# Performance work log

Measured on AMD Instinct MI355X. Metric: run time of the kernel, lower is better.

## Reference

```python
import jax, jax.numpy as jnp
import numpy as np

EPS = 1e-12  # matches torch euclidean_dist clamp(min=1e-12)


def _euclidean_dist(a, b):
    # pairwise sqrt distances: [N, M]
    d2 = (jnp.sum(a * a, axis=1)[:, None]
          + jnp.sum(b * b, axis=1)[None, :]
          - 2.0 * (a @ b.T))
    return jnp.sqrt(jnp.clip(d2, EPS))


def setup_inputs() -> dict:
    key = jax.random.key(0)
    k1, k2, k3 = jax.random.split(key, 3)
    B, I, E, C = 131072, 512, 128, 64
    x = jax.random.normal(k1, (B, I), dtype=jnp.float32)
    y = jax.random.randint(k2, (B,), 0, C)  # class labels
    W = jax.random.normal(k3, (E, I), dtype=jnp.float32) * 0.02
    b = jnp.zeros((E,), dtype=jnp.float32)
    centroid = jnp.zeros((C, E), dtype=jnp.float32)
    return {"x": x, "y": y, "W": W, "b": b, "centroid": centroid}


def reference(x, y, W, b, centroid):
    # linear projection: [B, E]
    out = x @ W.T + b
    C = centroid.shape[0]
    # fused per-class masked mean (segment mean). flag[i]==0 always in the
    # original module, so the executed update is centroid[i] += mean_i.
    sums = jax.ops.segment_sum(out, y, num_segments=C)            # [C, E]
    counts = jax.ops.segment_sum(jnp.ones(y.shape, out.dtype), y,
                                 num_segments=C)                   # [C]
    means = sums / counts[:, None]
    new_centroid = centroid + means
    # only the final loop iteration's proto_dist / dist survive
    proto_dist = jnp.exp(-0.5 * _euclidean_dist(new_centroid, new_centroid))
    dist = _euclidean_dist(out, new_centroid)                      # [B, C]
    return jax.nn.sigmoid(jnp.exp(-0.5 * dist)), proto_dist
```

## Files before the change

### kernel.cpp

```cpp
#include <hip/hip_runtime.h>
#include <math.h>


typedef __bf16 bf16;
typedef bf16  bf16x2 __attribute__((ext_vector_type(2)));
typedef bf16  bf16x4 __attribute__((ext_vector_type(4)));
typedef bf16  bf16x8 __attribute__((ext_vector_type(8)));
typedef float f32x4  __attribute__((ext_vector_type(4)));

#define B_ROWS 131072
#define K_DIM  512
#define E_DIM  128
#define C_CLS  64

#define BM 128
#define BK 64

#define SEG_BLOCKS 512
#define ROWS_PER_SEG (B_ROWS / SEG_BLOCKS)

#define DIST_BLOCKS (B_ROWS / 128)
#define PROTO_BLOCKS 16

__global__ __launch_bounds__(256, 2)
void gemm_kernel(const float* __restrict__ x, const float* __restrict__ W,
                 const float* __restrict__ bias, bf16* __restrict__ outb,
                 float* __restrict__ rnorm)
{
    __shared__ bf16 As[2][BM * BK];
    __shared__ bf16 Bs[2][BM * BK];
    __shared__ float lr[BM];

    const int t    = threadIdx.x;
    const int lane = t & 63;
    const int w    = t >> 6;
    const int wr   = w >> 1;
    const int wc   = w & 1;
    const int fr   = lane & 15;
    const int fq   = lane >> 4;
    const long blockRow = (long)blockIdx.x * BM;

    const int srow = t >> 4;
    const int scol = (t & 15) * 4;

    f32x4 acc[4][4] = {};
    f32x4 va[8], vb[8];

    const float* xg = x + blockRow * K_DIM;
    if (t < BM) lr[t] = 0.f;

    #pragma unroll
    for (int r = 0; r < 8; ++r) {
        int row = r * 16 + srow;
        va[r] = *(const f32x4*)(xg + (long)row * K_DIM + scol);
        vb[r] = *(const f32x4*)(W  + (long)row * K_DIM + scol);
    }
    #pragma unroll
    for (int r = 0; r < 8; ++r) {
        int row = r * 16 + srow;
        bf16x4 pa = { (bf16)va[r].x, (bf16)va[r].y, (bf16)va[r].z, (bf16)va[r].w };
        bf16x4 pb = { (bf16)vb[r].x, (bf16)vb[r].y, (bf16)vb[r].z, (bf16)vb[r].w };
        int byte = row * (BK * 2) + ((scol * 2) ^ ((row & 7) << 4));
        *(bf16x4*)((char*)As[0] + byte) = pa;
        *(bf16x4*)((char*)Bs[0] + byte) = pb;
    }
    __syncthreads();

    for (int kti = 0; kti < K_DIM / BK; ++kti) {
        const int p = kti & 1;
        if (kti < K_DIM / BK - 1) {
            const int kt = (kti + 1) * BK;
            #pragma unroll
            for (int r = 0; r < 8; ++r) {
                int row = r * 16 + srow;
                va[r] = *(const f32x4*)(xg + (long)row * K_DIM + kt + scol);
                vb[r] = *(const f32x4*)(W  + (long)row * K_DIM + kt + scol);
            }
        }
        const bf16* Ap = As[p];
        const bf16* Bp = Bs[p];
        #pragma unroll
        for (int kk = 0; kk < 2; ++kk) {
            bf16x8 af[4], bg[4];
            #pragma unroll
            for (int m = 0; m < 4; ++m) {
                int row  = wr * 64 + m * 16 + fr;
                int byte = row * (BK * 2) + (((kk * 32 + fq * 8) * 2) ^ ((row & 7) << 4));
                af[m] = *(const bf16x8*)((const char*)Ap + byte);
            }
            #pragma unroll
            for (int n = 0; n < 4; ++n) {
                int row  = wc * 64 + n * 16 + fr;
                int byte = row * (BK * 2) + (((kk * 32 + fq * 8) * 2) ^ ((row & 7) << 4));
                bg[n] = *(const bf16x8*)((const char*)Bp + byte);
            }
            #pragma unroll
            for (int m = 0; m < 4; ++m)
                #pragma unroll
                for (int n = 0; n < 4; ++n)
                    acc[m][n] = __builtin_amdgcn_mfma_f32_16x16x32_bf16(
                        af[m], bg[n], acc[m][n], 0, 0, 0);
        }
        if (kti < K_DIM / BK - 1) {
            #pragma unroll
            for (int r = 0; r < 8; ++r) {
                int row = r * 16 + srow;
                bf16x4 pa = { (bf16)va[r].x, (bf16)va[r].y, (bf16)va[r].z, (bf16)va[r].w };
                bf16x4 pb = { (bf16)vb[r].x, (bf16)vb[r].y, (bf16)vb[r].z, (bf16)vb[r].w };
                int byte = row * (BK * 2) + ((scol * 2) ^ ((row & 7) << 4));
                *(bf16x4*)((char*)As[p ^ 1] + byte) = pa;
                *(bf16x4*)((char*)Bs[p ^ 1] + byte) = pb;
            }
            __syncthreads();
        }
    }

    float bvv[4];
    #pragma unroll
    for (int n = 0; n < 4; ++n) bvv[n] = bias[wc * 64 + n * 16 + fr];

    #pragma unroll
    for (int m = 0; m < 4; ++m) {
        #pragma unroll
        for (int j = 0; j < 4; ++j) {
            long grow = blockRow + wr * 64 + m * 16 + fq * 4 + j;
            float s = 0.f;
            #pragma unroll
            for (int n = 0; n < 4; ++n) {
                float v = acc[m][n][j] + bvv[n];
                outb[grow * E_DIM + wc * 64 + n * 16 + fr] = (bf16)v;
                s += v * v;
            }
            s += __shfl_xor(s, 1); s += __shfl_xor(s, 2);
            s += __shfl_xor(s, 4); s += __shfl_xor(s, 8);
            if (fr == 0) atomicAdd(&lr[wr * 64 + m * 16 + fq * 4 + j], s);
        }
    }
    __syncthreads();
    if (t < BM) rnorm[blockRow + t] = lr[t];
}

__global__ __launch_bounds__(256)
void segsum_kernel(const bf16* __restrict__ outb, const int* __restrict__ y,
                   float* __restrict__ pw, float* __restrict__ pc)
{
    __shared__ float lsum[C_CLS * E_DIM];
    __shared__ float lcnt[C_CLS];
    __shared__ int   ly[ROWS_PER_SEG];
    const int t = threadIdx.x;
    for (int i = t; i < C_CLS * E_DIM; i += 256) lsum[i] = 0.f;
    if (t < C_CLS) lcnt[t] = 0.f;
    const long base = (long)blockIdx.x * ROWS_PER_SEG;
    if (t < ROWS_PER_SEG) ly[t] = y[base + t];
    __syncthreads();
    const int w = t >> 6, lane = t & 63;
    #pragma unroll 4
    for (int i = w; i < ROWS_PER_SEG; i += 4) {
        int cls = ly[i];
        bf16x2 v = *(const bf16x2*)(outb + (base + i) * E_DIM + lane * 2);
        atomicAdd(&lsum[cls * E_DIM + lane * 2 + 0], (float)v[0]);
        atomicAdd(&lsum[cls * E_DIM + lane * 2 + 1], (float)v[1]);
        if (lane == 0) atomicAdd(&lcnt[cls], 1.f);
    }
    __syncthreads();
    for (int i = t; i < C_CLS * E_DIM; i += 256)
        pw[(long)blockIdx.x * (C_CLS * E_DIM) + i] = lsum[i];
    if (t < C_CLS) pc[blockIdx.x * C_CLS + t] = lcnt[t];
}

__global__ __launch_bounds__(256)
void reduce_kernel(const float* __restrict__ pw, float* __restrict__ sums)
{
    __shared__ float red[256];
    const int t = threadIdx.x;
    const int idx = blockIdx.x * 32 + (t & 31);
    const int js  = t >> 5;
    float s = 0.f;
    #pragma unroll 8
    for (int j = js * 64; j < js * 64 + 64; ++j)
        s += pw[(long)j * (C_CLS * E_DIM) + idx];
    red[t] = s;
    __syncthreads();
    if (t < 32) {
        float r = red[t];
        #pragma unroll
        for (int k = 1; k < 8; ++k) r += red[t + 32 * k];
        sums[blockIdx.x * 32 + t] = r;
    }
}

__global__ __launch_bounds__(256)
void centroid_kernel(const float* __restrict__ sums, const float* __restrict__ pc,
                     const float* __restrict__ centroid0,
                     float* __restrict__ cent, float* __restrict__ cnorm)
{
    __shared__ float red[256];
    const int c = blockIdx.x;
    const int t = threadIdx.x;
    float s = pc[t * C_CLS + c] + pc[(t + 256) * C_CLS + c];
    red[t] = s;
    __syncthreads();
    #pragma unroll
    for (int st = 128; st > 0; st >>= 1) {
        if (t < st) red[t] += red[t + st];
        __syncthreads();
    }
    const float cnt = red[0];
    __syncthreads();
    float v = 0.f;
    if (t < E_DIM) {
        v = centroid0[c * E_DIM + t] + sums[c * E_DIM + t] / cnt;
        cent[c * E_DIM + t] = v;
    }
    red[t] = v * v;
    __syncthreads();
    #pragma unroll
    for (int st = 64; st > 0; st >>= 1) {
        if (t < st) red[t] += red[t + st];
        __syncthreads();
    }
    if (t == 0) cnorm[c] = red[0];
}

__global__ __launch_bounds__(256, 4)
void dist_kernel(const bf16* __restrict__ outb, const float* __restrict__ cent,
                 const float* __restrict__ cnorm, const float* __restrict__ rnorm,
                 float* __restrict__ out0, float* __restrict__ proto)
{
    __shared__ float smemf[C_CLS * 129 + C_CLS + 128];
    const int t = threadIdx.x;

    if (blockIdx.x >= DIST_BLOCKS) {
        float* scf   = smemf;
        float* pnorm = smemf + C_CLS * 129;
        for (int idx = t; idx < C_CLS * E_DIM; idx += 256)
            scf[(idx >> 7) * 129 + (idx & 127)] = cent[idx];
        if (t < C_CLS) pnorm[t] = cnorm[t];
        __syncthreads();
        int p = (blockIdx.x - DIST_BLOCKS) * 256 + t;
        int i = p >> 6, j = p & 63;
        float d = 0.f;
        #pragma unroll 4
        for (int e = 0; e < E_DIM; ++e)
            d += scf[i * 129 + e] * scf[j * 129 + e];
        float d2 = pnorm[i] + pnorm[j] - 2.f * d;
        proto[p] = __expf(-0.5f * sqrtf(fmaxf(d2, 1e-12f)));
        return;
    }

    bf16*  Cs     = (bf16*)smemf;
    float* snorm  = smemf + C_CLS * 129;
    float* srnorm = snorm + C_CLS;
    {
        int srw = t >> 5;
        int scl = (t & 31) * 4;
        #pragma unroll
        for (int r = 0; r < 8; ++r) {
            int row = r * 8 + srw;
            f32x4 v = *(const f32x4*)(cent + row * E_DIM + scl);
            bf16x4 pv = { (bf16)v.x, (bf16)v.y, (bf16)v.z, (bf16)v.w };
            int byte = row * (E_DIM * 2) + ((scl * 2) ^ ((row & 7) << 4));
            *(bf16x4*)((char*)Cs + byte) = pv;
        }
        if (t < C_CLS) snorm[t] = cnorm[t];
        if (t < 32) ((f32x4*)srnorm)[t] =
            ((const f32x4*)(rnorm + (long)blockIdx.x * 128))[t];
    }
    const int lane = t & 63;
    const int w    = t >> 6;
    const int fr   = lane & 15;
    const int fq   = lane >> 4;
    const long blkrow = (long)blockIdx.x * 128;
    f32x4 acc[2][4] = {};
    __syncthreads();
    #pragma unroll
    for (int kt = 0; kt < 4; ++kt) {
        bf16x8 af[2];
        #pragma unroll
        for (int m = 0; m < 2; ++m) {
            long row = blkrow + w * 32 + m * 16 + fr;
            af[m] = *(const bf16x8*)(outb + row * E_DIM + kt * 32 + fq * 8);
        }
        #pragma unroll
        for (int n = 0; n < 4; ++n) {
            int row  = n * 16 + fr;
            int byte = row * (E_DIM * 2) + (((kt * 32 + fq * 8) * 2) ^ ((row & 7) << 4));
            bf16x8 bq = *(const bf16x8*)((const char*)Cs + byte);
            acc[0][n] = __builtin_amdgcn_mfma_f32_16x16x32_bf16(af[0], bq, acc[0][n], 0, 0, 0);
            acc[1][n] = __builtin_amdgcn_mfma_f32_16x16x32_bf16(af[1], bq, acc[1][n], 0, 0, 0);
        }
    }
    #pragma unroll
    for (int m = 0; m < 2; ++m) {
        #pragma unroll
        for (int n = 0; n < 4; ++n) {
            int gcol = n * 16 + fr;
            float cn = snorm[gcol];
            #pragma unroll
            for (int j = 0; j < 4; ++j) {
                int lrow = w * 32 + m * 16 + fq * 4 + j;
                float d2 = srnorm[lrow] + cn - 2.f * acc[m][n][j];
                float dist = sqrtf(fmaxf(d2, 1e-12f));
                float ez = __expf(-0.5f * dist);
                out0[(blkrow + lrow) * C_CLS + gcol] = 1.f / (1.f + __expf(-ez));
            }
        }
    }
}

extern "C" void kernel_launch(void* const* d_in, const int* in_sizes, int n_in,
                              void* d_out, int out_size, void* d_ws, size_t ws_size,
                              hipStream_t stream)
{
    const float* x         = (const float*)d_in[0];
    const int*   y         = (const int*)d_in[1];
    const float* W         = (const float*)d_in[2];
    const float* bias      = (const float*)d_in[3];
    const float* centroid0 = (const float*)d_in[4];

    bf16*  outb  = (bf16*)d_ws;
    float* rnorm = (float*)((char*)d_ws + (size_t)B_ROWS * E_DIM * 2);
    float* pw    = rnorm + B_ROWS;
    float* pc    = pw + (long)SEG_BLOCKS * C_CLS * E_DIM;
    float* sums  = pc + SEG_BLOCKS * C_CLS;
    float* cent  = sums + C_CLS * E_DIM;
    float* cnorm = cent + C_CLS * E_DIM;

    float* out0  = (float*)d_out;
    float* proto = out0 + (long)B_ROWS * C_CLS;

    gemm_kernel    <<<B_ROWS / BM, 256, 0, stream>>>(x, W, bias, outb, rnorm);
    segsum_kernel  <<<SEG_BLOCKS, 256, 0, stream>>>(outb, y, pw, pc);
    reduce_kernel  <<<(C_CLS * E_DIM) / 32, 256, 0, stream>>>(pw, sums);
    centroid_kernel<<<C_CLS, 256, 0, stream>>>(sums, pc, centroid0, cent, cnorm);
    dist_kernel    <<<DIST_BLOCKS + PROTO_BLOCKS, 256, 0, stream>>>(
        outb, cent, cnorm, rnorm, out0, proto);
}
```

Measured before the change: 194.7 us.

## Fuse all stages into one persistent kernel with software grid barriers

Replaces the five-kernel pipeline with a single persistent kernel of 512 blocks that runs GEMM, segment sum, reduction, centroid update and distance stages, separated by atomic-counter grid barriers. Each block handles two GEMM tiles and two distance tiles, and the centroid and norm computation is done redundantly in every block. The aim is to remove launch gaps and the small serial kernels. The risks are that GEMM occupancy falls to 512 blocks (a 64KB static LDS allocation), that barrier spinning adds cost, and that progress depends on all blocks being co-resident.

Result: slower. 416.8 us (+114.1%).

```diff
diff --git a/kernel.cpp b/kernel.cpp
--- a/kernel.cpp
+++ b/kernel.cpp
@@ -16,294 +16,282 @@
 #define BM 128
 #define BK 64
 
-#define SEG_BLOCKS 512
-#define ROWS_PER_SEG (B_ROWS / SEG_BLOCKS)
-
-#define DIST_BLOCKS (B_ROWS / 128)
-#define PROTO_BLOCKS 16
+#define GRID 512
+#define ROWS_PER_SEG (B_ROWS / GRID)
+
+__device__ __forceinline__ void grid_sync(unsigned* bar, unsigned target)
+{
+    __syncthreads();
+    if (threadIdx.x == 0) {
+        __threadfence();
+        atomicAdd(bar, 1u);
+        while (atomicAdd(bar, 0u) < target)
+            __builtin_amdgcn_s_sleep(16);
+    }
+    __syncthreads();
+    __threadfence();
+}
 
 __global__ __launch_bounds__(256, 2)
-void gemm_kernel(const float* __restrict__ x, const float* __restrict__ W,
-                 const float* __restrict__ bias, bf16* __restrict__ outb,
-                 float* __restrict__ rnorm)
+void mega_kernel(const float* __restrict__ x, const int* __restrict__ y,
+                 const float* __restrict__ W, const float* __restrict__ bias,
+                 const float* __restrict__ centroid0,
+                 bf16* __restrict__ outb, float* __restrict__ rnorm,
+                 float* __restrict__ pw, float* __restrict__ pc,
+                 float* __restrict__ sums, float* __restrict__ cntg,
+                 float* __restrict__ out0, float* __restrict__ proto,
+                 unsigned* __restrict__ bar)
 {
-    __shared__ bf16 As[2][BM * BK];
-    __shared__ bf16 Bs[2][BM * BK];
-    __shared__ float lr[BM];
-
+    __shared__ __align__(16) char smem[65536];
     const int t    = threadIdx.x;
     const int lane = t & 63;
     const int w    = t >> 6;
-    const int wr   = w >> 1;
-    const int wc   = w & 1;
-    const int fr   = lane & 15;
-    const int fq   = lane >> 4;
-    const long blockRow = (long)blockIdx.x * BM;
-
-    const int srow = t >> 4;
-    const int scol = (t & 15) * 4;
-
-    f32x4 acc[4][4] = {};
-    f32x4 va[8], vb[8];
-
-    const float* xg = x + blockRow * K_DIM;
-    if (t < BM) lr[t] = 0.f;
-
-    #pragma unroll
-    for (int r = 0; r < 8; ++r) {
-        int row = r * 16 + srow;
-        va[r] = *(const f32x4*)(xg + (long)row * K_DIM + scol);
-        vb[r] = *(const f32x4*)(W  + (long)row * K_DIM + scol);
-    }
-    #pragma unroll
-    for (int r = 0; r < 8; ++r) {
-        int row = r * 16 + srow;
-        bf16x4 pa = { (bf16)va[r].x, (bf16)va[r].y, (bf16)va[r].z, (bf16)va[r].w };
-        bf16x4 pb = { (bf16)vb[r].x, (bf16)vb[r].y, (bf16)vb[r].z, (bf16)vb[r].w };
-        int byte = row * (BK * 2) + ((scol * 2) ^ ((row & 7) << 4));
-        *(bf16x4*)((char*)As[0] + byte) = pa;
-        *(bf16x4*)((char*)Bs[0] + byte) = pb;
-    }
-    __syncthreads();
-
-    for (int kti = 0; kti < K_DIM / BK; ++kti) {
-        const int p = kti & 1;
-        if (kti < K_DIM / BK - 1) {
-            const int kt = (kti + 1) * BK;
+
+    {
+        bf16* As = (bf16*)smem;
+        bf16* Bs = (bf16*)(smem + 32768);
+        const int wr = w >> 1, wc = w & 1;
+        const int fr = lane & 15, fq = lane >> 4;
+        const int srow = t >> 4;
+        const int scol = (t & 15) * 4;
+
+        for (int rep = 0; rep < 2; ++rep) {
+            const int  tile = blockIdx.x + rep * GRID;
+            const long blockRow = (long)tile * BM;
+            const float* xg = x + blockRow * K_DIM;
+            f32x4 acc[4][4] = {};
+            f32x4 va[8], vb[8];
+
+            __syncthreads();
             #pragma unroll
             for (int r = 0; r < 8; ++r) {
                 int row = r * 16 + srow;
-                va[r] = *(const f32x4*)(xg + (long)row * K_DIM + kt + scol);
-                vb[r] = *(const f32x4*)(W  + (long)row * K_DIM + kt + scol);
-            }
-        }
-        const bf16* Ap = As[p];
-        const bf16* Bp = Bs[p];
-        #pragma unroll
-        for (int kk = 0; kk < 2; ++kk) {
-            bf16x8 af[4], bg[4];
-            #pragma unroll
-            for (int m = 0; m < 4; ++m) {
-                int row  = wr * 64 + m * 16 + fr;
-                int byte = row * (BK * 2) + (((kk * 32 + fq * 8) * 2) ^ ((row & 7) << 4));
-                af[m] = *(const bf16x8*)((const char*)Ap + byte);
-            }
-            #pragma unroll
-            for (int n = 0; n < 4; ++n) {
-                int row  = wc * 64 + n * 16 + fr;
-                int byte = row * (BK * 2) + (((kk * 32 + fq * 8) * 2) ^ ((row & 7) << 4));
-                bg[n] = *(const bf16x8*)((const char*)Bp + byte);
-            }
-            #pragma unroll
-            for (int m = 0; m < 4; ++m)
-                #pragma unroll
-                for (int n = 0; n < 4; ++n)
-                    acc[m][n] = __builtin_amdgcn_mfma_f32_16x16x32_bf16(
-                        af[m], bg[n], acc[m][n], 0, 0, 0);
-        }
-        if (kti < K_DIM / BK - 1) {
+                va[r] = *(const f32x4*)(xg + (long)row * K_DIM + scol);
+                vb[r] = *(const f32x4*)(W  + (long)row * K_DIM + scol);
+            }
             #pragma unroll
             for (int r = 0; r < 8; ++r) {
                 int row = r * 16 + srow;
                 bf16x4 pa = { (bf16)va[r].x, (bf16)va[r].y, (bf16)va[r].z, (bf16)va[r].w };
                 bf16x4 pb = { (bf16)vb[r].x, (bf16)vb[r].y, (bf16)vb[r].z, (bf16)vb[r].w };
                 int byte = row * (BK * 2) + ((scol * 2) ^ ((row & 7) << 4));
-                *(bf16x4*)((char*)As[p ^ 1] + byte) = pa;
-                *(bf16x4*)((char*)Bs[p ^ 1] + byte) = pb;
-            }
-            __syncthreads();
-        }
-    }
-
-    float bvv[4];
-    #pragma unroll
-    for (int n = 0; n < 4; ++n) bvv[n] = bias[wc * 64 + n * 16 + fr];
-
-    #pragma unroll
-    for (int m = 0; m < 4; ++m) {
-        #pragma unroll
-        for (int j = 0; j < 4; ++j) {
-            long grow = blockRow + wr * 64 + m * 16 + fq * 4 + j;
-            float s = 0.f;
-            #pragma unroll
-            for (int n = 0; n < 4; ++n) {
-                float v = acc[m][n][j] + bvv[n];
-                outb[grow * E_DIM + wc * 64 + n * 16 + fr] = (bf16)v;
-                s += v * v;
-            }
-            s += __shfl_xor(s, 1); s += __shfl_xor(s, 2);
-            s += __shfl_xor(s, 4); s += __shfl_xor(s, 8);
-            if (fr == 0) atomicAdd(&lr[wr * 64 + m * 16 + fq * 4 + j], s);
-        }
-    }
-    __syncthreads();
-    if (t < BM) rnorm[blockRow + t] = lr[t];
-}
-
-__global__ __launch_bounds__(256)
-void segsum_kernel(const bf16* __restrict__ outb, const int* __restrict__ y,
-                   float* __restrict__ pw, float* __restrict__ pc)
-{
-    __shared__ float lsum[C_CLS * E_DIM];
-    __shared__ float lcnt[C_CLS];
-    __shared__ int   ly[ROWS_PER_SEG];
-    const int t = threadIdx.x;
-    for (int i = t; i < C_CLS * E_DIM; i += 256) lsum[i] = 0.f;
-    if (t < C_CLS) lcnt[t] = 0.f;
-    const long base = (long)blockIdx.x * ROWS_PER_SEG;
-    if (t < ROWS_PER_SEG) ly[t] = y[base + t];
-    __syncthreads();
-    const int w = t >> 6, lane = t & 63;
-    #pragma unroll 4
-    for (int i = w; i < ROWS_PER_SEG; i += 4) {
-        int cls = ly[i];
-        bf16x2 v = *(const bf16x2*)(outb + (base + i) * E_DIM + lane * 2);
-        atomicAdd(&lsum[cls * E_DIM + lane * 2 + 0], (float)v[0]);
-        atomicAdd(&lsum[cls * E_DIM + lane * 2 + 1], (float)v[1]);
-        if (lane == 0) atomicAdd(&lcnt[cls], 1.f);
-    }
-    __syncthreads();
-    for (int i = t; i < C_CLS * E_DIM; i += 256)
-        pw[(long)blockIdx.x * (C_CLS * E_DIM) + i] = lsum[i];
-    if (t < C_CLS) pc[blockIdx.x * C_CLS + t] = lcnt[t];
-}
-
-__global__ __launch_bounds__(256)
-void reduce_kernel(const float* __restrict__ pw, float* __restrict__ sums)
-{
-    __shared__ float red[256];
-    const int t = threadIdx.x;
-    const int idx = blockIdx.x * 32 + (t & 31);
-    const int js  = t >> 5;
-    float s = 0.f;
-    #pragma unroll 8
-    for (int j = js * 64; j < js * 64 + 64; ++j)
-        s += pw[(long)j * (C_CLS * E_DIM) + idx];
-    red[t] = s;
-    __syncthreads();
-    if (t < 32) {
-        float r = red[t];
-        #pragma unroll
-        for (int k = 1; k < 8; ++k) r += red[t + 32 * k];
-        sums[blockIdx.x * 32 + t] = r;
-    }
-}
-
-__global__ __launch_bounds__(256)
-void centroid_kernel(const float* __restrict__ sums, const float* __restrict__ pc,
-                     const float* __restrict__ centroid0,
-                     float* __restrict__ cent, float* __restrict__ cnorm)
-{
-    __shared__ float red[256];
-    const int c = blockIdx.x;
-    const int t = threadIdx.x;
-    float s = pc[t * C_CLS + c] + pc[(t + 256) * C_CLS + c];
-    red[t] = s;
-    __syncthreads();
-    #pragma unroll
-    for (int st = 128; st > 0; st >>= 1) {
-        if (t < st) red[t] += red[t + st];
-        __syncthreads();
-    }
-    const float cnt = red[0];
-    __syncthreads();
-    float v = 0.f;
-    if (t < E_DIM) {
-        v = centroid0[c * E_DIM + t] + sums[c * E_DIM + t] / cnt;
-        cent[c * E_DIM + t] = v;
-    }
-    red[t] = v * v;
-    __syncthreads();
-    #pragma unroll
-    for (int st = 64; st > 0; st >>= 1) {
-        if (t < st) red[t] += red[t + st];
-        __syncthreads();
-    }
-    if (t == 0) cnorm[c] = red[0];
-}
-
-__global__ __launch_bounds__(256, 4)
-void dist_kernel(const bf16* __restrict__ outb, const float* __restrict__ cent,
-                 const float* __restrict__ cnorm, const float* __restrict__ rnorm,
-                 float* __restrict__ out0, float* __restrict__ proto)
-{
-    __shared__ float smemf[C_CLS * 129 + C_CLS + 128];
-    const int t = threadIdx.x;
-
-    if (blockIdx.x >= DIST_BLOCKS) {
-        float* scf   = smemf;
-        float* pnorm = smemf + C_CLS * 129;
-        for (int idx = t; idx < C_CLS * E_DIM; idx += 256)
-            scf[(idx >> 7) * 129 + (idx & 127)] = cent[idx];
-        if (t < C_CLS) pnorm[t] = cnorm[t];
-        __syncthreads();
-        int p = (blockIdx.x - DIST_BLOCKS) * 256 + t;
-        int i = p >> 6, j = p & 63;
-        float d = 0.f;
+                *(bf16x4*)((char*)As + byte) = pa;
+                *(bf16x4*)((char*)Bs + byte) = pb;
+            }
+            __syncthreads();
+
+            for (int kti = 0; kti < K_DIM / BK; ++kti) {
+                const int p = kti & 1;
+                if (kti < K_DIM / BK - 1) {
+                    const int kt = (kti + 1) * BK;
+                    #pragma unroll
+                    for (int r = 0; r < 8; ++r) {
+                        int row = r * 16 + srow;
+                        va[r] = *(const f32x4*)(xg + (long)row * K_DIM + kt + scol);
+                        vb[r] = *(const f32x4*)(W  + (long)row * K_DIM + kt + scol);
+                    }
+                }
+                const char* Ap = (const char*)As + p * 16384;
+                const char* Bp = (const char*)Bs + p * 16384;
+                #pragma unroll
+                for (int kk = 0; kk < 2; ++kk) {
+                    bf16x8 af[4], bg[4];
+                    #pragma unroll
+                    for (int m = 0; m < 4; ++m) {
+                        int row  = wr * 64 + m * 16 + fr;
+                        int byte = row * (BK * 2) + (((kk * 32 + fq * 8) * 2) ^ ((row & 7) << 4));
+                        af[m] = *(const bf16x8*)(Ap + byte);
+                    }
+                    #pragma unroll
+                    for (int n = 0; n < 4; ++n) {
+                        int row  = wc * 64 + n * 16 + fr;
+                        int byte = row * (BK * 2) + (((kk * 32 + fq * 8) * 2) ^ ((row & 7) << 4));
+                        bg[n] = *(const bf16x8*)(Bp + byte);
+                    }
+                    #pragma unroll
+                    for (int m = 0; m < 4; ++m)
+                        #pragma unroll
+                        for (int n = 0; n < 4; ++n)
+                            acc[m][n] = __builtin_amdgcn_mfma_f32_16x16x32_bf16(
+                                af[m], bg[n], acc[m][n], 0, 0, 0);
+                }
+                if (kti < K_DIM / BK - 1) {
+                    #pragma unroll
+                    for (int r = 0; r < 8; ++r) {
+                        int row = r * 16 + srow;
+                        bf16x4 pa = { (bf16)va[r].x, (bf16)va[r].y, (bf16)va[r].z, (bf16)va[r].w };
+                        bf16x4 pb = { (bf16)vb[r].x, (bf16)vb[r].y, (bf16)vb[r].z, (bf16)vb[r].w };
+                        int byte = row * (BK * 2) + ((scol * 2) ^ ((row & 7) << 4));
+                        *(bf16x4*)((char*)As + (p ^ 1) * 16384 + byte) = pa;
+                        *(bf16x4*)((char*)Bs + (p ^ 1) * 16384 + byte) = pb;
+                    }
+                    __syncthreads();
+                }
+            }
+
+            __syncthreads();
+            float* lr = (float*)smem;
+            if (t < BM) lr[t] = 0.f;
+            __syncthreads();
+            float bvv[4];
+            #pragma unroll
+            for (int n = 0; n < 4; ++n) bvv[n] = bias[wc * 64 + n * 16 + fr];
+            #pragma unroll
+            for (int m = 0; m < 4; ++m) {
+                #pragma unroll
+                for (int j = 0; j < 4; ++j) {
+                    long grow = blockRow + wr * 64 + m * 16 + fq * 4 + j;
+                    float s = 0.f;
+                    #pragma unroll
+                    for (int n = 0; n < 4; ++n) {
+                        float v = acc[m][n][j] + bvv[n];
+                        outb[grow * E_DIM + wc * 64 + n * 16 + fr] = (bf16)v;
+                        s += v * v;
+                    }
+                    s += __shfl_xor(s, 1); s += __shfl_xor(s, 2);
+                    s += __shfl_xor(s, 4); s += __shfl_xor(s, 8);
+                    if (fr == 0) atomicAdd(&lr[wr * 64 + m * 16 + fq * 4 + j], s);
+                }
+            }
+            __syncthreads();
+            if (t < BM) rnorm[blockRow + t] = lr[t];
+        }
+    }
+    grid_sync(bar, GRID);
+
+    {
+        float* lsum = (float*)smem;
+        float* lcnt = (float*)(smem + 32768);
+        int*   ly   = (int*)(smem + 33024);
+        for (int i = t; i < C_CLS * E_DIM; i += 256) lsum[i] = 0.f;
+        if (t < C_CLS) lcnt[t] = 0.f;
+        const long base = (long)blockIdx.x * ROWS_PER_SEG;
+        if (t < ROWS_PER_SEG) ly[t] = y[base + t];
+        __syncthreads();
         #pragma unroll 4
-        for (int e = 0; e < E_DIM; ++e)
-            d += scf[i * 129 + e] * scf[j * 129 + e];
-        float d2 = pnorm[i] + pnorm[j] - 2.f * d;
-        proto[p] = __expf(-0.5f * sqrtf(fmaxf(d2, 1e-12f)));
-        return;
-    }
-
-    bf16*  Cs     = (bf16*)smemf;
-    float* snorm  = smemf + C_CLS * 129;
-    float* srnorm = snorm + C_CLS;
+        for (int i = w; i < ROWS_PER_SEG; i += 4) {
+            int cls = ly[i];
+            bf16x2 v = *(const bf16x2*)(outb + (base + i) * E_DIM + lane * 2);
+            atomicAdd(&lsum[cls * E_DIM + lane * 2 + 0], (float)v[0]);
+            atomicAdd(&lsum[cls * E_DIM + lane * 2 + 1], (float)v[1]);
+            if (lane == 0) atomicAdd(&lcnt[cls], 1.f);
+        }
+        __syncthreads();
+        for (int i = t; i < C_CLS * E_DIM; i += 256)
+            pw[(long)blockIdx.x * (C_CLS * E_DIM) + i] = lsum[i];
+        if (t < C_CLS) pc[blockIdx.x * C_CLS + t] = lcnt[t];
+    }
+    grid_sync(bar, 2 * GRID);
+
     {
-        int srw = t >> 5;
-        int scl = (t & 31) * 4;
-        #pragma unroll
-        for (int r = 0; r < 8; ++r) {
-            int row = r * 8 + srw;
-            f32x4 v = *(const f32x4*)(cent + row * E_DIM + scl);
-            bf16x4 pv = { (bf16)v.x, (bf16)v.y, (bf16)v.z, (bf16)v.w };
-            int byte = row * (E_DIM * 2) + ((scl * 2) ^ ((row & 7) << 4));
-            *(bf16x4*)((char*)Cs + byte) = pv;
-        }
-        if (t < C_CLS) snorm[t] = cnorm[t];
-        if (t < 32) ((f32x4*)srnorm)[t] =
-            ((const f32x4*)(rnorm + (long)blockIdx.x * 128))[t];
-    }
-    const int lane = t & 63;
-    const int w    = t >> 6;
-    const int fr   = lane & 15;
-    const int fq   = lane >> 4;
-    const long blkrow = (long)blockIdx.x * 128;
-    f32x4 acc[2][4] = {};
-    __syncthreads();
-    #pragma unroll
-    for (int kt = 0; kt < 4; ++kt) {
-        bf16x8 af[2];
-        #pragma unroll
-        for (int m = 0; m < 2; ++m) {
-            long row = blkrow + w * 32 + m * 16 + fr;
-            af[m] = *(const bf16x8*)(outb + row * E_DIM + kt * 32 + fq * 8);
-        }
-        #pragma unroll
-        for (int n = 0; n < 4; ++n) {
-            int row  = n * 16 + fr;
-            int byte = row * (E_DIM * 2) + (((kt * 32 + fq * 8) * 2) ^ ((row & 7) << 4));
-            bf16x8 bq = *(const bf16x8*)((const char*)Cs + byte);
-            acc[0][n] = __builtin_amdgcn_mfma_f32_16x16x32_bf16(af[0], bq, acc[0][n], 0, 0, 0);
-            acc[1][n] = __builtin_amdgcn_mfma_f32_16x16x32_bf16(af[1], bq, acc[1][n], 0, 0, 0);
-        }
-    }
-    #pragma unroll
-    for (int m = 0; m < 2; ++m) {
-        #pragma unroll
-        for (int n = 0; n < 4; ++n) {
-            int gcol = n * 16 + fr;
-            float cn = snorm[gcol];
-            #pragma unroll
-            for (int j = 0; j < 4; ++j) {
-                int lrow = w * 32 + m * 16 + fq * 4 + j;
-                float d2 = srnorm[lrow] + cn - 2.f * acc[m][n][j];
-                float dist = sqrtf(fmaxf(d2, 1e-12f));
-                float ez = __expf(-0.5f * dist);
-                out0[(blkrow + lrow) * C_CLS + gcol] = 1.f / (1.f + __expf(-ez));
-            }
+        float* scr = (float*)smem;
+        const int i16 = t & 15, slice = t >> 4;
+        const int idx = blockIdx.x * 16 + i16;
+        float s = 0.f;
+        #pragma unroll 8
+        for (int j = slice * 32; j < slice * 32 + 32; ++j)
+            s += pw[(long)j * (C_CLS * E_DIM) + idx];
+        scr[slice * 16 + i16] = s;
+        __syncthreads();
+        if (t < 16) {
+            float r = 0.f;
+            #pragma unroll
+            for (int k = 0; k < 16; ++k) r += scr[k * 16 + t];
+            sums[blockIdx.x * 16 + t] = r;
+        }
+        if (blockIdx.x < C_CLS) {
+            __syncthreads();
+            int c = blockIdx.x;
+            scr[t] = pc[t * C_CLS + c] + pc[(t + 256) * C_CLS + c];
+            __syncthreads();
+            for (int st = 128; st > 0; st >>= 1) {
+                if (t < st) scr[t] += scr[t + st];
+                __syncthreads();
+            }
+            if (t == 0) cntg[c] = scr[0];
+        }
+    }
+    grid_sync(bar, 3 * GRID);
+
+    {
+        float* centf  = (float*)smem;
+        float* cnormS = (float*)(smem + 33024);
+        bf16*  Cs     = (bf16*)(smem + 33280);
+        float* srn    = (float*)(smem + 49664);
+        float* scr2   = (float*)(smem + 50176);
+
+        for (int i = t; i < C_CLS * E_DIM; i += 256) {
+            int cc = i >> 7, e = i & 127;
+            float v = centroid0[i] + sums[i] / cntg[cc];
+            centf[cc * 129 + e] = v;
+            int byte = cc * 256 + ((e * 2) ^ ((cc & 7) << 4));
+            *(bf16*)((char*)Cs + byte) = (bf16)v;
+        }
+        __syncthreads();
+        {
+            int c = t >> 2, q = t & 3;
+            float sSum = 0.f;
+            #pragma unroll 8
+            for (int e = q * 32; e < q * 32 + 32; ++e) {
+                float v = centf[c * 129 + e];
+                sSum += v * v;
+            }
+            scr2[t] = sSum;
+        }
+        __syncthreads();
+        if (t < C_CLS)
+            cnormS[t] = scr2[4 * t] + scr2[4 * t + 1] + scr2[4 * t + 2] + scr2[4 * t + 3];
+
+        const int fr = lane & 15, fq = lane >> 4;
+        for (int rep = 0; rep < 2; ++rep) {
+            const long blkrow = (long)(blockIdx.x + rep * GRID) * 128;
+            __syncthreads();
+            if (t < 32) ((f32x4*)srn)[t] = ((const f32x4*)(rnorm + blkrow))[t];
+            __syncthreads();
+            f32x4 acc[2][4] = {};
+            #pragma unroll
+            for (int kt = 0; kt < 4; ++kt) {
+                bf16x8 af[2];
+                #pragma unroll
+                for (int m = 0; m < 2; ++m) {
+                    long row = blkrow + w * 32 + m * 16 + fr;
+                    af[m] = *(const bf16x8*)(outb + row * E_DIM + kt * 32 + fq * 8);
+                }
+                #pragma unroll
+                for (int n = 0; n < 4; ++n) {
+                    int row  = n * 16 + fr;
+                    int byte = row * (E_DIM * 2) + (((kt * 32 + fq * 8) * 2) ^ ((row & 7) << 4));
+                    bf16x8 bq = *(const bf16x8*)((const char*)Cs + byte);
+                    acc[0][n] = __builtin_amdgcn_mfma_f32_16x16x32_bf16(af[0], bq, acc[0][n], 0, 0, 0);
+                    acc[1][n] = __builtin_amdgcn_mfma_f32_16x16x32_bf16(af[1], bq, acc[1][n], 0, 0, 0);
+                }
+            }
+            #pragma unroll
+            for (int m = 0; m < 2; ++m) {
+                #pragma unroll
+                for (int n = 0; n < 4; ++n) {
+                    int gcol = n * 16 + fr;
+                    float cn = cnormS[gcol];
+                    #pragma unroll
+                    for (int j = 0; j < 4; ++j) {
+                        int lrow = w * 32 + m * 16 + fq * 4 + j;
+                        float d2 = srn[lrow] + cn - 2.f * acc[m][n][j];
+                        float dist = sqrtf(fmaxf(d2, 1e-12f));
+                        float ez = __expf(-0.5f * dist);
+                        out0[(blkrow + lrow) * C_CLS + gcol] = 1.f / (1.f + __expf(-ez));
+                    }
+                }
+            }
+        }
+        if (blockIdx.x < 16) {
+            int p = blockIdx.x * 256 + t;
+            int i = p >> 6, j = p & 63;
+            float d = 0.f;
+            #pragma unroll 4
+            for (int e = 0; e < E_DIM; ++e)
+                d += centf[i * 129 + e] * centf[j * 129 + e];
+            float d2 = cnormS[i] + cnormS[j] - 2.f * d;
+            proto[p] = __expf(-0.5f * sqrtf(fmaxf(d2, 1e-12f)));
         }
     }
 }
@@ -318,21 +306,20 @@
     const float* bias      = (const float*)d_in[3];
     const float* centroid0 = (const float*)d_in[4];
 
-    bf16*  outb  = (bf16*)d_ws;
-    float* rnorm = (float*)((char*)d_ws + (size_t)B_ROWS * E_DIM * 2);
-    float* pw    = rnorm + B_ROWS;
-    float* pc    = pw + (long)SEG_BLOCKS * C_CLS * E_DIM;
-    float* sums  = pc + SEG_BLOCKS * C_CLS;
-    float* cent  = sums + C_CLS * E_DIM;
-    float* cnorm = cent + C_CLS * E_DIM;
+    char* ws = (char*)d_ws;
+    bf16*  outb  = (bf16*)ws;
+    float* rnorm = (float*)(ws + 33554432);
+    float* pw    = (float*)(ws + 34078720);
+    float* pc    = (float*)(ws + 50855936);
+    float* sums  = (float*)(ws + 50987008);
+    float* cntg  = (float*)(ws + 51019776);
+    unsigned* bar = (unsigned*)(ws + 51020032);
 
     float* out0  = (float*)d_out;
     float* proto = out0 + (long)B_ROWS * C_CLS;
 
-    gemm_kernel    <<<B_ROWS / BM, 256, 0, stream>>>(x, W, bias, outb, rnorm);
-    segsum_kernel  <<<SEG_BLOCKS, 256, 0, stream>>>(outb, y, pw, pc);
-    reduce_kernel  <<<(C_CLS * E_DIM) / 32, 256, 0, stream>>>(pw, sums);
-    centroid_kernel<<<C_CLS, 256, 0, stream>>>(sums, pc, centroid0, cent, cnorm);
-    dist_kernel    <<<DIST_BLOCKS + PROTO_BLOCKS, 256, 0, stream>>>(
-        outb, cent, cnorm, rnorm, out0, proto);
+    hipMemsetAsync(bar, 0, 64, stream);
+    hipLaunchKernelGGL(mega_kernel, dim3(GRID), dim3(256), 0, stream,
+                       x, y, W, bias, centroid0,
+                       outb, rnorm, pw, pc, sums, cntg, out0, proto, bar);
 }
```

## Fuse class segment-sum into GEMM epilogue and merge reduction into centroid kernel

Applied to the files above, without the earlier changes.

The GEMM kernel now processes two row tiles per block and, in its epilogue, accumulates per-class sums and counts into shared memory, writing per-tile partials. This removes the separate segsum pass that re-read the projected activations, plus the reduce kernel. The centroid kernel now reduces all 1024 partials directly. In exchange, partial-buffer writes double, the final reduction runs on only 64 blocks, and shared-memory atomics in the epilogue may contend.

Measured after the change: 299.2 us. 1.54x slower.

```diff
diff --git a/kernel.cpp b/kernel.cpp
--- a/kernel.cpp
+++ b/kernel.cpp
@@ -3,7 +3,6 @@
 
 
 typedef __bf16 bf16;
-typedef bf16  bf16x2 __attribute__((ext_vector_type(2)));
 typedef bf16  bf16x4 __attribute__((ext_vector_type(4)));
 typedef bf16  bf16x8 __attribute__((ext_vector_type(8)));
 typedef float f32x4  __attribute__((ext_vector_type(4)));
@@ -16,210 +15,201 @@
 #define BM 128
 #define BK 64
 
-#define SEG_BLOCKS 512
-#define ROWS_PER_SEG (B_ROWS / SEG_BLOCKS)
+#define GRID_A 512
+#define N_TILES 1024
 
 #define DIST_BLOCKS (B_ROWS / 128)
 #define PROTO_BLOCKS 16
 
 __global__ __launch_bounds__(256, 2)
-void gemm_kernel(const float* __restrict__ x, const float* __restrict__ W,
-                 const float* __restrict__ bias, bf16* __restrict__ outb,
-                 float* __restrict__ rnorm)
+void gemmseg_kernel(const float* __restrict__ x, const int* __restrict__ y,
+                    const float* __restrict__ W, const float* __restrict__ bias,
+                    bf16* __restrict__ outb, float* __restrict__ rnorm,
+                    float* __restrict__ pw, float* __restrict__ pc)
 {
-    __shared__ bf16 As[2][BM * BK];
-    __shared__ bf16 Bs[2][BM * BK];
-    __shared__ float lr[BM];
+    __shared__ __align__(16) char smem[67072];
+    bf16*  As   = (bf16*)smem;
+    bf16*  Bs   = (bf16*)(smem + 32768);
+    int*   ly   = (int*)(smem + 65536);
+    float* lr   = (float*)(smem + 66560);
+    float* lsum = (float*)smem;
+    float* lcnt = (float*)(smem + 32768);
 
     const int t    = threadIdx.x;
     const int lane = t & 63;
     const int w    = t >> 6;
-    const int wr   = w >> 1;
-    const int wc   = w & 1;
-    const int fr   = lane & 15;
-    const int fq   = lane >> 4;
-    const long blockRow = (long)blockIdx.x * BM;
-
+    const int wr   = w >> 1, wc = w & 1;
+    const int fr   = lane & 15, fq = lane >> 4;
     const int srow = t >> 4;
     const int scol = (t & 15) * 4;
 
-    f32x4 acc[4][4] = {};
-    f32x4 va[8], vb[8];
-
-    const float* xg = x + blockRow * K_DIM;
-    if (t < BM) lr[t] = 0.f;
-
-    #pragma unroll
-    for (int r = 0; r < 8; ++r) {
-        int row = r * 16 + srow;
-        va[r] = *(const f32x4*)(xg + (long)row * K_DIM + scol);
-        vb[r] = *(const f32x4*)(W  + (long)row * K_DIM + scol);
-    }
-    #pragma unroll
-    for (int r = 0; r < 8; ++r) {
-        int row = r * 16 + srow;
-        bf16x4 pa = { (bf16)va[r].x, (bf16)va[r].y, (bf16)va[r].z, (bf16)va[r].w };
-        bf16x4 pb = { (bf16)vb[r].x, (bf16)vb[r].y, (bf16)vb[r].z, (bf16)vb[r].w };
-        int byte = row * (BK * 2) + ((scol * 2) ^ ((row & 7) << 4));
-        *(bf16x4*)((char*)As[0] + byte) = pa;
-        *(bf16x4*)((char*)Bs[0] + byte) = pb;
-    }
-    __syncthreads();
-
-    for (int kti = 0; kti < K_DIM / BK; ++kti) {
-        const int p = kti & 1;
-        if (kti < K_DIM / BK - 1) {
-            const int kt = (kti + 1) * BK;
-            #pragma unroll
-            for (int r = 0; r < 8; ++r) {
-                int row = r * 16 + srow;
-                va[r] = *(const f32x4*)(xg + (long)row * K_DIM + kt + scol);
-                vb[r] = *(const f32x4*)(W  + (long)row * K_DIM + kt + scol);
-            }
-        }
-        const bf16* Ap = As[p];
-        const bf16* Bp = Bs[p];
-        #pragma unroll
-        for (int kk = 0; kk < 2; ++kk) {
-            bf16x8 af[4], bg[4];
-            #pragma unroll
-            for (int m = 0; m < 4; ++m) {
-                int row  = wr * 64 + m * 16 + fr;
-                int byte = row * (BK * 2) + (((kk * 32 + fq * 8) * 2) ^ ((row & 7) << 4));
-                af[m] = *(const bf16x8*)((const char*)Ap + byte);
-            }
-            #pragma unroll
-            for (int n = 0; n < 4; ++n) {
-                int row  = wc * 64 + n * 16 + fr;
-                int byte = row * (BK * 2) + (((kk * 32 + fq * 8) * 2) ^ ((row & 7) << 4));
-                bg[n] = *(const bf16x8*)((const char*)Bp + byte);
-            }
-            #pragma unroll
-            for (int m = 0; m < 4; ++m)
-                #pragma unroll
-                for (int n = 0; n < 4; ++n)
-                    acc[m][n] = __builtin_amdgcn_mfma_f32_16x16x32_bf16(
-                        af[m], bg[n], acc[m][n], 0, 0, 0);
-        }
-        if (kti < K_DIM / BK - 1) {
-            #pragma unroll
-            for (int r = 0; r < 8; ++r) {
-                int row = r * 16 + srow;
-                bf16x4 pa = { (bf16)va[r].x, (bf16)va[r].y, (bf16)va[r].z, (bf16)va[r].w };
-                bf16x4 pb = { (bf16)vb[r].x, (bf16)vb[r].y, (bf16)vb[r].z, (bf16)vb[r].w };
-                int byte = row * (BK * 2) + ((scol * 2) ^ ((row & 7) << 4));
-                *(bf16x4*)((char*)As[p ^ 1] + byte) = pa;
-                *(bf16x4*)((char*)Bs[p ^ 1] + byte) = pb;
-            }
-            __syncthreads();
-        }
-    }
+    const long baseRow = (long)blockIdx.x * 256;
+    if (t < 256) ly[t] = y[baseRow + t];
 
     float bvv[4];
     #pragma unroll
     for (int n = 0; n < 4; ++n) bvv[n] = bias[wc * 64 + n * 16 + fr];
 
-    #pragma unroll
-    for (int m = 0; m < 4; ++m) {
-        #pragma unroll
-        for (int j = 0; j < 4; ++j) {
-            long grow = blockRow + wr * 64 + m * 16 + fq * 4 + j;
-            float s = 0.f;
+    for (int rep = 0; rep < 2; ++rep) {
+        const int  tile = blockIdx.x * 2 + rep;
+        const long blockRow = (long)tile * BM;
+        const float* xg = x + blockRow * K_DIM;
+        f32x4 acc[4][4] = {};
+        f32x4 va[8], vb[8];
+
+        __syncthreads();
+        #pragma unroll
+        for (int r = 0; r < 8; ++r) {
+            int row = r * 16 + srow;
+            va[r] = *(const f32x4*)(xg + (long)row * K_DIM + scol);
+            vb[r] = *(const f32x4*)(W  + (long)row * K_DIM + scol);
+        }
+        #pragma unroll
+        for (int r = 0; r < 8; ++r) {
+            int row = r * 16 + srow;
+            bf16x4 pa = { (bf16)va[r].x, (bf16)va[r].y, (bf16)va[r].z, (bf16)va[r].w };
+            bf16x4 pb = { (bf16)vb[r].x, (bf16)vb[r].y, (bf16)vb[r].z, (bf16)vb[r].w };
+            int byte = row * (BK * 2) + ((scol * 2) ^ ((row & 7) << 4));
+            *(bf16x4*)((char*)As + byte) = pa;
+            *(bf16x4*)((char*)Bs + byte) = pb;
+        }
+        __syncthreads();
+
+        for (int kti = 0; kti < K_DIM / BK; ++kti) {
+            const int p = kti & 1;
+            if (kti < K_DIM / BK - 1) {
+                const int kt = (kti + 1) * BK;
+                #pragma unroll
+                for (int r = 0; r < 8; ++r) {
+                    int row = r * 16 + srow;
+                    va[r] = *(const f32x4*)(xg + (long)row * K_DIM + kt + scol);
+                    vb[r] = *(const f32x4*)(W  + (long)row * K_DIM + kt + scol);
+                }
+            }
+            const char* Ap = (const char*)As + p * 16384;
+            const char* Bp = (const char*)Bs + p * 16384;
             #pragma unroll
-            for (int n = 0; n < 4; ++n) {
-                float v = acc[m][n][j] + bvv[n];
-                outb[grow * E_DIM + wc * 64 + n * 16 + fr] = (bf16)v;
-                s += v * v;
-            }
-            s += __shfl_xor(s, 1); s += __shfl_xor(s, 2);
-            s += __shfl_xor(s, 4); s += __shfl_xor(s, 8);
-            if (fr == 0) atomicAdd(&lr[wr * 64 + m * 16 + fq * 4 + j], s);
-        }
-    }
-    __syncthreads();
-    if (t < BM) rnorm[blockRow + t] = lr[t];
+            for (int kk = 0; kk < 2; ++kk) {
+                bf16x8 af[4], bg[4];
+                #pragma unroll
+                for (int m = 0; m < 4; ++m) {
+                    int row  = wr * 64 + m * 16 + fr;
+                    int byte = row * (BK * 2) + (((kk * 32 + fq * 8) * 2) ^ ((row & 7) << 4));
+                    af[m] = *(const bf16x8*)(Ap + byte);
+                }
+                #pragma unroll
+                for (int n = 0; n < 4; ++n) {
+                    int row  = wc * 64 + n * 16 + fr;
+                    int byte = row * (BK * 2) + (((kk * 32 + fq * 8) * 2) ^ ((row & 7) << 4));
+                    bg[n] = *(const bf16x8*)(Bp + byte);
+                }
+                #pragma unroll
+                for (int m = 0; m < 4; ++m)
+                    #pragma unroll
+                    for (int n = 0; n < 4; ++n)
+                        acc[m][n] = __builtin_amdgcn_mfma_f32_16x16x32_bf16(
+                            af[m], bg[n], acc[m][n], 0, 0, 0);
+            }
+            if (kti < K_DIM / BK - 1) {
+                #pragma unroll
+                for (int r = 0; r < 8; ++r) {
+                    int row = r * 16 + srow;
+                    bf16x4 pa = { (bf16)va[r].x, (bf16)va[r].y, (bf16)va[r].z, (bf16)va[r].w };
+                    bf16x4 pb = { (bf16)vb[r].x, (bf16)vb[r].y, (bf16)vb[r].z, (bf16)vb[r].w };
+                    int byte = row * (BK * 2) + ((scol * 2) ^ ((row & 7) << 4));
+                    *(bf16x4*)((char*)As + (p ^ 1) * 16384 + byte) = pa;
+                    *(bf16x4*)((char*)Bs + (p ^ 1) * 16384 + byte) = pb;
+                }
+                __syncthreads();
+            }
+        }
+
+        __syncthreads();
+        for (int i = t; i < C_CLS * E_DIM; i += 256) lsum[i] = 0.f;
+        if (t < C_CLS) lcnt[t] = 0.f;
+        if (t < BM)    lr[t]   = 0.f;
+        __syncthreads();
+
+        if (t < BM) atomicAdd(&lcnt[ly[rep * 128 + t]], 1.f);
+
+        #pragma unroll
+        for (int m = 0; m < 4; ++m) {
+            #pragma unroll
+            for (int j = 0; j < 4; ++j) {
+                int  lrow = wr * 64 + m * 16 + fq * 4 + j;
+                long grow = blockRow + lrow;
+                int  cls  = ly[rep * 128 + lrow];
+                float s = 0.f;
+                #pragma unroll
+                for (int n = 0; n < 4; ++n) {
+                    float v = acc[m][n][j] + bvv[n];
+                    outb[grow * E_DIM + wc * 64 + n * 16 + fr] = (bf16)v;
+                    s += v * v;
+                    atomicAdd(&lsum[cls * E_DIM + wc * 64 + n * 16 + fr], v);
+                }
+                s += __shfl_xor(s, 1); s += __shfl_xor(s, 2);
+                s += __shfl_xor(s, 4); s += __shfl_xor(s, 8);
+                if (fr == 0) atomicAdd(&lr[lrow], s);
+            }
+        }
+        __syncthreads();
+
+        for (int i = t; i < C_CLS * E_DIM; i += 256)
+            pw[(long)tile * (C_CLS * E_DIM) + i] = lsum[i];
+        if (t < C_CLS) pc[tile * C_CLS + t] = lcnt[t];
+        if (t < BM)    rnorm[blockRow + t]  = lr[t];
+    }
 }
 
 __global__ __launch_bounds__(256)
-void segsum_kernel(const bf16* __restrict__ outb, const int* __restrict__ y,
-                   float* __restrict__ pw, float* __restrict__ pc)
-{
-    __shared__ float lsum[C_CLS * E_DIM];
-    __shared__ float lcnt[C_CLS];
-    __shared__ int   ly[ROWS_PER_SEG];
-    const int t = threadIdx.x;
-    for (int i = t; i < C_CLS * E_DIM; i += 256) lsum[i] = 0.f;
-    if (t < C_CLS) lcnt[t] = 0.f;
-    const long base = (long)blockIdx.x * ROWS_PER_SEG;
-    if (t < ROWS_PER_SEG) ly[t] = y[base + t];
-    __syncthreads();
-    const int w = t >> 6, lane = t & 63;
-    #pragma unroll 4
-    for (int i = w; i < ROWS_PER_SEG; i += 4) {
-        int cls = ly[i];
-        bf16x2 v = *(const bf16x2*)(outb + (base + i) * E_DIM + lane * 2);
-        atomicAdd(&lsum[cls * E_DIM + lane * 2 + 0], (float)v[0]);
-        atomicAdd(&lsum[cls * E_DIM + lane * 2 + 1], (float)v[1]);
-        if (lane == 0) atomicAdd(&lcnt[cls], 1.f);
-    }
-    __syncthreads();
-    for (int i = t; i < C_CLS * E_DIM; i += 256)
-        pw[(long)blockIdx.x * (C_CLS * E_DIM) + i] = lsum[i];
-    if (t < C_CLS) pc[blockIdx.x * C_CLS + t] = lcnt[t];
-}
-
-__global__ __launch_bounds__(256)
-void reduce_kernel(const float* __restrict__ pw, float* __restrict__ sums)
-{
-    __shared__ float red[256];
-    const int t = threadIdx.x;
-    const int idx = blockIdx.x * 32 + (t & 31);
-    const int js  = t >> 5;
-    float s = 0.f;
-    #pragma unroll 8
-    for (int j = js * 64; j < js * 64 + 64; ++j)
-        s += pw[(long)j * (C_CLS * E_DIM) + idx];
-    red[t] = s;
-    __syncthreads();
-    if (t < 32) {
-        float r = red[t];
-        #pragma unroll
-        for (int k = 1; k < 8; ++k) r += red[t + 32 * k];
-        sums[blockIdx.x * 32 + t] = r;
-    }
-}
-
-__global__ __launch_bounds__(256)
-void centroid_kernel(const float* __restrict__ sums, const float* __restrict__ pc,
+void centroid_kernel(const float* __restrict__ pw, const float* __restrict__ pc,
                      const float* __restrict__ centroid0,
                      float* __restrict__ cent, float* __restrict__ cnorm)
 {
-    __shared__ float red[256];
+    __shared__ float scr[256];
+    __shared__ float sumv[128];
     const int c = blockIdx.x;
     const int t = threadIdx.x;
-    float s = pc[t * C_CLS + c] + pc[(t + 256) * C_CLS + c];
-    red[t] = s;
-    __syncthreads();
-    #pragma unroll
-    for (int st = 128; st > 0; st >>= 1) {
-        if (t < st) red[t] += red[t + st];
-        __syncthreads();
-    }
-    const float cnt = red[0];
-    __syncthreads();
-    float v = 0.f;
-    if (t < E_DIM) {
-        v = centroid0[c * E_DIM + t] + sums[c * E_DIM + t] / cnt;
-        cent[c * E_DIM + t] = v;
-    }
-    red[t] = v * v;
-    __syncthreads();
-    #pragma unroll
-    for (int st = 64; st > 0; st >>= 1) {
-        if (t < st) red[t] += red[t + st];
-        __syncthreads();
-    }
-    if (t == 0) cnorm[c] = red[0];
+
+    {
+        float s = 0.f;
+        #pragma unroll
+        for (int k = 0; k < 4; ++k) s += pc[(t * 4 + k) * C_CLS + c];
+        scr[t] = s;
+        __syncthreads();
+        #pragma unroll
+        for (int st = 128; st > 0; st >>= 1) {
+            if (t < st) scr[t] += scr[t + st];
+            __syncthreads();
+        }
+    }
+    const float cnt = scr[0];
+    __syncthreads();
+
+    {
+        const int e = t & 127, half = t >> 7;
+        float s = 0.f;
+        for (int j = half * 512; j < half * 512 + 512; ++j)
+            s += pw[(long)j * (C_CLS * E_DIM) + c * E_DIM + e];
+        scr[t] = s;
+        __syncthreads();
+        if (t < 128) {
+            float v = centroid0[c * E_DIM + t] + (scr[t] + scr[t + 128]) / cnt;
+            cent[c * E_DIM + t] = v;
+            sumv[t] = v * v;
+        }
+    }
+    __syncthreads();
+    if (t < 64) sumv[t] += sumv[t + 64];
+    __syncthreads();
+    if (t < 32) sumv[t] += sumv[t + 32];
+    __syncthreads();
+    if (t == 0) {
+        float s = 0.f;
+        #pragma unroll
+        for (int k = 0; k < 32; ++k) s += sumv[k];
+        cnorm[c] = s;
+    }
 }
 
 __global__ __launch_bounds__(256, 4)
@@ -318,21 +308,19 @@
     const float* bias      = (const float*)d_in[3];
     const float* centroid0 = (const float*)d_in[4];
 
-    bf16*  outb  = (bf16*)d_ws;
-    float* rnorm = (float*)((char*)d_ws + (size_t)B_ROWS * E_DIM * 2);
-    float* pw    = rnorm + B_ROWS;
-    float* pc    = pw + (long)SEG_BLOCKS * C_CLS * E_DIM;
-    float* sums  = pc + SEG_BLOCKS * C_CLS;
-    float* cent  = sums + C_CLS * E_DIM;
-    float* cnorm = cent + C_CLS * E_DIM;
+    char* ws = (char*)d_ws;
+    bf16*  outb  = (bf16*)ws;
+    float* rnorm = (float*)(ws + 33554432);
+    float* pw    = (float*)(ws + 34078720);
+    float* pc    = (float*)(ws + 67633152);
+    float* cent  = (float*)(ws + 67895296);
+    float* cnorm = (float*)(ws + 67928064);
 
     float* out0  = (float*)d_out;
     float* proto = out0 + (long)B_ROWS * C_CLS;
 
-    gemm_kernel    <<<B_ROWS / BM, 256, 0, stream>>>(x, W, bias, outb, rnorm);
-    segsum_kernel  <<<SEG_BLOCKS, 256, 0, stream>>>(outb, y, pw, pc);
-    reduce_kernel  <<<(C_CLS * E_DIM) / 32, 256, 0, stream>>>(pw, sums);
-    centroid_kernel<<<C_CLS, 256, 0, stream>>>(sums, pc, centroid0, cent, cnorm);
+    gemmseg_kernel <<<GRID_A, 256, 0, stream>>>(x, y, W, bias, outb, rnorm, pw, pc);
+    centroid_kernel<<<C_CLS, 256, 0, stream>>>(pw, pc, centroid0, cent, cnorm);
     dist_kernel    <<<DIST_BLOCKS + PROTO_BLOCKS, 256, 0, stream>>>(
         outb, cent, cnorm, rnorm, out0, proto);
 }
```
